# Kernel tuning notes

Hardware: AMD Instinct MI355X
Metric: run time of the kernel (lower is better)

## Reference

```python
import jax, jax.numpy as jnp
import numpy as np

N = 262144        # examples
N_RULES = 128     # weak labeling functions
D_L = 128         # extra feature dim of x_l
NHIDDEN = 256
NCLASS = 10
NFEAT = N_RULES + D_L


def setup_inputs() -> dict:
    key = jax.random.key(0)
    k1, k2, k3, k4 = jax.random.split(key, 4)
    # weak-rule votes: -1 = abstain, 0..NCLASS-1 = class vote (stored as float, as in torch)
    x_lf = jax.random.randint(k1, (N, N_RULES), -1, NCLASS).astype(jnp.float32)
    x_l = jax.random.normal(k2, (N, D_L), dtype=jnp.float32)
    W1 = jax.random.normal(k3, (NFEAT, NHIDDEN), dtype=jnp.float32) / np.sqrt(NFEAT).astype(np.float32)
    b1 = jnp.zeros((NHIDDEN,), jnp.float32)
    W2 = jax.random.normal(k4, (NHIDDEN, N_RULES), dtype=jnp.float32) / np.sqrt(NHIDDEN).astype(np.float32)
    b2 = jnp.zeros((N_RULES,), jnp.float32)
    return {"x_lf": x_lf, "x_l": x_l, "W1": W1, "b1": b1, "W2": W2, "b2": b2}


def reference(x_lf, x_l, W1, b1, W2, b2):
    # MLP attention scores over rules
    x = jnp.concatenate([x_lf, x_l], axis=1)            # (N, NFEAT)
    z = jnp.tanh(x @ W1 + b1) @ W2 + b2                 # (N, N_RULES)
    score = jax.nn.softmax(z, axis=1)                   # (N, N_RULES)
    mask = (x_lf >= 0).astype(score.dtype)
    coverage_score = score * mask                       # (N, N_RULES)
    # bucket-sum of scores by voted class (single-pass scatter-add instead of
    # the original O(nclass) masked-reduction loop); abstains (-1) -> bucket NCLASS, dropped
    idx = jnp.where(x_lf >= 0, x_lf.astype(jnp.int32), NCLASS)  # (N, N_RULES)
    score_matrix = jax.vmap(
        lambda s, i: jax.ops.segment_sum(s, i, num_segments=NCLASS + 1)
    )(score, idx)[:, :NCLASS]                           # (N, NCLASS)
    softmax_new_y = jax.nn.log_softmax(score_matrix, axis=1)
    return softmax_new_y, coverage_score
```

## Files before the change

### kernel.cpp

```cpp
#include <hip/hip_runtime.h>
#include <hip/hip_bf16.h>

#define NRULES 128
#define NH 256
#define NC 10
#define NF 256
#define BM 128

typedef __attribute__((ext_vector_type(8))) __bf16 bf16x8;
typedef __attribute__((ext_vector_type(4))) __bf16 bf16x4;
typedef __attribute__((ext_vector_type(4))) float f32x4;
typedef __attribute__((ext_vector_type(4))) int i32x4;

static __device__ __forceinline__ unsigned int f2bf_bits(float f) {
    unsigned int u = __float_as_uint(f);
    u += 0x7fffu + ((u >> 16) & 1u);
    return u >> 16;
}

static __device__ __forceinline__ float tanh_fast(float x) {
    float xc = fminf(fmaxf(x, -15.f), 15.f);
    float e = __expf(2.f * xc);
    return 1.f - 2.f * __builtin_amdgcn_rcpf(e + 1.f);
}

__global__ __launch_bounds__(256) void prep_transpose(
    const float* __restrict__ W1, const float* __restrict__ W2,
    unsigned short* __restrict__ W1T, unsigned short* __restrict__ W2T)
{
    __shared__ float tile[64][65];
    const int b = blockIdx.x;
    const float* src;
    unsigned short* dst;
    int sstride;
    if (b < 16) {
        int ti = b >> 2, tj = b & 3;
        src = W1 + ti * 64 * 256 + tj * 64;  sstride = 256;
        dst = W1T + tj * 64 * 256 + ti * 64;
    } else {
        int bb = b - 16;
        int ti = bb >> 1, tj = bb & 1;
        src = W2 + ti * 64 * 128 + tj * 64;  sstride = 128;
        dst = W2T + tj * 64 * 256 + ti * 64;
    }
    const int t = threadIdx.x;
    #pragma unroll
    for (int i = 0; i < 4; ++i) {
        int idx = i * 256 + t;
        int r = idx >> 4, c4 = (idx & 15) * 4;
        f32x4 v = *(const f32x4*)(src + r * sstride + c4);
        tile[r][c4 + 0] = v.x; tile[r][c4 + 1] = v.y;
        tile[r][c4 + 2] = v.z; tile[r][c4 + 3] = v.w;
    }
    __syncthreads();
    #pragma unroll
    for (int i = 0; i < 2; ++i) {
        int idx = i * 256 + t;
        int rr = idx >> 3, cc = (idx & 7) * 8;
        i32x4 pk;
        #pragma unroll
        for (int j = 0; j < 4; ++j) {
            unsigned int lo = f2bf_bits(tile[cc + 2 * j][rr]);
            unsigned int hi = f2bf_bits(tile[cc + 2 * j + 1][rr]);
            pk[j] = (int)(lo | (hi << 16));
        }
        *(i32x4*)(dst + rr * 256 + cc) = pk;
    }
}

__global__ __launch_bounds__(512, 4) void fused_mlp_attn(
    const float* __restrict__ x_lf, const float* __restrict__ x_l,
    const float* __restrict__ b1, const float* __restrict__ b2,
    const unsigned short* __restrict__ W1T, const unsigned short* __restrict__ W2T,
    float* __restrict__ out0, float* __restrict__ out1)
{
    __shared__ __align__(16) unsigned char smem[BM * 512 + BM * 68];
    unsigned char* Xs = smem;
    unsigned char* Vs = smem + BM * 512;

    const int tid = threadIdx.x;
    const long e0 = (long)blockIdx.x * BM;

    #pragma unroll
    for (int i = 0; i < 8; ++i) {
        int idx = i * 512 + tid;
        int e = idx >> 5;
        int c = idx & 31;
        const float* src = (c < 16) ? (x_lf + (e0 + e) * 128 + c * 8)
                                    : (x_l  + (e0 + e) * 128 + (c - 16) * 8);
        f32x4 a  = *(const f32x4*)src;
        f32x4 bq = *(const f32x4*)(src + 4);
        bf16x8 pk;
        pk[0] = (__bf16)a.x;  pk[1] = (__bf16)a.y;
        pk[2] = (__bf16)a.z;  pk[3] = (__bf16)a.w;
        pk[4] = (__bf16)bq.x; pk[5] = (__bf16)bq.y;
        pk[6] = (__bf16)bq.z; pk[7] = (__bf16)bq.w;
        *(bf16x8*)(Xs + e * 512 + ((c ^ (e & 7)) << 4)) = pk;
        if (c < 16) {
            unsigned int v = 0;
            v |= (unsigned int)((int)a.x  + 1);
            v |= (unsigned int)((int)a.y  + 1) << 4;
            v |= (unsigned int)((int)a.z  + 1) << 8;
            v |= (unsigned int)((int)a.w  + 1) << 12;
            v |= (unsigned int)((int)bq.x + 1) << 16;
            v |= (unsigned int)((int)bq.y + 1) << 20;
            v |= (unsigned int)((int)bq.z + 1) << 24;
            v |= (unsigned int)((int)bq.w + 1) << 28;
            *(unsigned int*)(Vs + e * 68 + c * 4) = v;
        }
    }
    __syncthreads();

    const int wv  = tid >> 6;
    const int lane = tid & 63;
    const int q   = lane >> 4;
    const int l15 = lane & 15;

    const int hb = wv * 32;
    f32x4 acc[2][8];
    #pragma unroll
    for (int mt = 0; mt < 2; ++mt)
        #pragma unroll
        for (int nt = 0; nt < 8; ++nt)
            acc[mt][nt] = (f32x4){0.f, 0.f, 0.f, 0.f};

    for (int kk = 0; kk < 8; ++kk) {
        const int k = kk * 32 + q * 8;
        bf16x8 af[2];
        #pragma unroll
        for (int mt = 0; mt < 2; ++mt)
            af[mt] = *(const bf16x8*)(W1T + (hb + mt * 16 + l15) * 256 + k);
        const int cc = kk * 4 + q;
        bf16x8 bfq[8];
        #pragma unroll
        for (int nt = 0; nt < 8; ++nt) {
            int e = nt * 16 + l15;
            bfq[nt] = *(const bf16x8*)(Xs + e * 512 + ((cc ^ (e & 7)) << 4));
        }
        #pragma unroll
        for (int mt = 0; mt < 2; ++mt)
            #pragma unroll
            for (int nt = 0; nt < 8; ++nt)
                acc[mt][nt] = __builtin_amdgcn_mfma_f32_16x16x32_bf16(
                    af[mt], bfq[nt], acc[mt][nt], 0, 0, 0);
    }

    #pragma unroll
    for (int mt = 0; mt < 2; ++mt) {
        f32x4 bv = *(const f32x4*)(b1 + hb + mt * 16 + q * 4);
        #pragma unroll
        for (int nt = 0; nt < 8; ++nt)
            #pragma unroll
            for (int j = 0; j < 4; ++j)
                acc[mt][nt][j] = tanh_fast(acc[mt][nt][j] + bv[j]);
    }

    __syncthreads();

    #pragma unroll
    for (int mt = 0; mt < 2; ++mt) {
        int h = hb + mt * 16 + q * 4;
        int c16 = h >> 3;
        int sub = (h & 4) << 1;
        #pragma unroll
        for (int nt = 0; nt < 8; ++nt) {
            int e = nt * 16 + l15;
            bf16x4 d;
            d[0] = (__bf16)acc[mt][nt][0]; d[1] = (__bf16)acc[mt][nt][1];
            d[2] = (__bf16)acc[mt][nt][2]; d[3] = (__bf16)acc[mt][nt][3];
            *(bf16x4*)(Xs + e * 512 + ((c16 ^ (e & 7)) << 4) + sub) = d;
        }
    }
    __syncthreads();

    const int eb = wv * 16;
    f32x4 acc2[8];
    #pragma unroll
    for (int mt = 0; mt < 8; ++mt)
        acc2[mt] = (f32x4){0.f, 0.f, 0.f, 0.f};

    for (int kk = 0; kk < 8; ++kk) {
        const int k = kk * 32 + q * 8;
        bf16x8 af2[8];
        #pragma unroll
        for (int mt = 0; mt < 8; ++mt)
            af2[mt] = *(const bf16x8*)(W2T + (mt * 16 + l15) * 256 + k);
        const int cc = kk * 4 + q;
        int e = eb + l15;
        bf16x8 bf2 = *(const bf16x8*)(Xs + e * 512 + ((cc ^ (e & 7)) << 4));
        #pragma unroll
        for (int mt = 0; mt < 8; ++mt)
            acc2[mt] = __builtin_amdgcn_mfma_f32_16x16x32_bf16(
                af2[mt], bf2, acc2[mt], 0, 0, 0);
    }

    {
        const int e = eb + l15;

        #pragma unroll
        for (int mt = 0; mt < 8; ++mt) {
            f32x4 bv = *(const f32x4*)(b2 + mt * 16 + q * 4);
            acc2[mt] += bv;
        }

        int vt[8];
        #pragma unroll
        for (int mt = 0; mt < 8; ++mt)
            vt[mt] = *(const unsigned short*)(Vs + e * 68 + mt * 8 + q * 2);

        float m = -3.4e38f;
        #pragma unroll
        for (int mt = 0; mt < 8; ++mt)
            #pragma unroll
            for (int j = 0; j < 4; ++j)
                m = fmaxf(m, acc2[mt][j]);
        m = fmaxf(m, __shfl_xor(m, 16));
        m = fmaxf(m, __shfl_xor(m, 32));

        float s = 0.f;
        #pragma unroll
        for (int mt = 0; mt < 8; ++mt)
            #pragma unroll
            for (int j = 0; j < 4; ++j) {
                float p = __expf(acc2[mt][j] - m);
                acc2[mt][j] = p;
                s += p;
            }
        s += __shfl_xor(s, 16);
        s += __shfl_xor(s, 32);
        const float inv = __builtin_amdgcn_rcpf(s);

        float bucket[NC];
        #pragma unroll
        for (int c = 0; c < NC; ++c) bucket[c] = 0.f;

        #pragma unroll
        for (int mt = 0; mt < 8; ++mt) {
            int u = vt[mt];
            f32x4 cov;
            #pragma unroll
            for (int j = 0; j < 4; ++j) {
                float sc = acc2[mt][j] * inv;
                int v = (u >> (4 * j)) & 15;
                cov[j] = (v != 0) ? sc : 0.f;
                #pragma unroll
                for (int c = 0; c < NC; ++c)
                    bucket[c] += (v == c + 1) ? sc : 0.f;
            }
            *(f32x4*)(out1 + (e0 + e) * 128 + mt * 16 + q * 4) = cov;
        }

        #pragma unroll
        for (int c = 0; c < NC; ++c) {
            bucket[c] += __shfl_xor(bucket[c], 16);
            bucket[c] += __shfl_xor(bucket[c], 32);
        }

        float m10 = bucket[0];
        #pragma unroll
        for (int c = 1; c < NC; ++c) m10 = fmaxf(m10, bucket[c]);
        float se = 0.f;
        #pragma unroll
        for (int c = 0; c < NC; ++c) se += __expf(bucket[c] - m10);
        const float lse = m10 + __logf(se);

        if (q == 0) {
            float* o = out0 + (e0 + e) * 10;
            #pragma unroll
            for (int c = 0; c < NC; ++c) o[c] = bucket[c] - lse;
        }
    }
}

extern "C" void kernel_launch(void* const* d_in, const int* in_sizes, int n_in,
                              void* d_out, int out_size, void* d_ws, size_t ws_size,
                              hipStream_t stream)
{
    const float* x_lf = (const float*)d_in[0];
    const float* x_l  = (const float*)d_in[1];
    const float* W1   = (const float*)d_in[2];
    const float* b1   = (const float*)d_in[3];
    const float* W2   = (const float*)d_in[4];
    const float* b2   = (const float*)d_in[5];
    const int n = in_sizes[0] / NRULES;
    float* out0 = (float*)d_out;
    float* out1 = out0 + (long)n * NC;
    unsigned short* W1T = (unsigned short*)d_ws;
    unsigned short* W2T = W1T + NH * NF;

    prep_transpose<<<24, 256, 0, stream>>>(W1, W2, W1T, W2T);
    fused_mlp_attn<<<n / BM, 512, 0, stream>>>(x_lf, x_l, b1, b2, W1T, W2T,
                                               out0, out1);
}
```

Before: 479.0 us.

## Stage coverage output through LDS and bucket scores with shared-memory atomics

```diff
diff --git a/kernel.cpp b/kernel.cpp
--- a/kernel.cpp
+++ b/kernel.cpp
@@ -74,13 +74,21 @@
     const unsigned short* __restrict__ W1T, const unsigned short* __restrict__ W2T,
     float* __restrict__ out0, float* __restrict__ out1)
 {
-    __shared__ __align__(16) unsigned char smem[BM * 512 + BM * 68];
+    __shared__ __align__(16) unsigned char smem[BM * 512 + BM * 68 + BM * 40];
     unsigned char* Xs = smem;
     unsigned char* Vs = smem + BM * 512;
+    float* lbuck = (float*)(smem + BM * 512 + BM * 68);
 
     const int tid = threadIdx.x;
     const long e0 = (long)blockIdx.x * BM;
 
+    #pragma unroll
+    for (int i = 0; i < 3; ++i) {
+        int idx = i * 512 + tid;
+        if (idx < BM * 10) lbuck[idx] = 0.f;
+    }
+
+    f32x4 ra[8], rb[8];
     #pragma unroll
     for (int i = 0; i < 8; ++i) {
         int idx = i * 512 + tid;
@@ -88,8 +96,15 @@
         int c = idx & 31;
         const float* src = (c < 16) ? (x_lf + (e0 + e) * 128 + c * 8)
                                     : (x_l  + (e0 + e) * 128 + (c - 16) * 8);
-        f32x4 a  = *(const f32x4*)src;
-        f32x4 bq = *(const f32x4*)(src + 4);
+        ra[i] = *(const f32x4*)src;
+        rb[i] = *(const f32x4*)(src + 4);
+    }
+    #pragma unroll
+    for (int i = 0; i < 8; ++i) {
+        int idx = i * 512 + tid;
+        int e = idx >> 5;
+        int c = idx & 31;
+        f32x4 a = ra[i], bq = rb[i];
         bf16x8 pk;
         pk[0] = (__bf16)a.x;  pk[1] = (__bf16)a.y;
         pk[2] = (__bf16)a.z;  pk[3] = (__bf16)a.w;
@@ -194,9 +209,8 @@
                 af2[mt], bf2, acc2[mt], 0, 0, 0);
     }
 
+    const int e = eb + l15;
     {
-        const int e = eb + l15;
-
         #pragma unroll
         for (int mt = 0; mt < 8; ++mt) {
             f32x4 bv = *(const f32x4*)(b2 + mt * 16 + q * 4);
@@ -230,45 +244,48 @@
         s += __shfl_xor(s, 32);
         const float inv = __builtin_amdgcn_rcpf(s);
 
-        float bucket[NC];
-        #pragma unroll
-        for (int c = 0; c < NC; ++c) bucket[c] = 0.f;
-
         #pragma unroll
         for (int mt = 0; mt < 8; ++mt) {
             int u = vt[mt];
-            f32x4 cov;
             #pragma unroll
             for (int j = 0; j < 4; ++j) {
                 float sc = acc2[mt][j] * inv;
                 int v = (u >> (4 * j)) & 15;
-                cov[j] = (v != 0) ? sc : 0.f;
-                #pragma unroll
-                for (int c = 0; c < NC; ++c)
-                    bucket[c] += (v == c + 1) ? sc : 0.f;
+                acc2[mt][j] = (v != 0) ? sc : 0.f;
+                if (v != 0) atomicAdd(&lbuck[e * 10 + v - 1], sc);
             }
-            *(f32x4*)(out1 + (e0 + e) * 128 + mt * 16 + q * 4) = cov;
-        }
-
-        #pragma unroll
-        for (int c = 0; c < NC; ++c) {
-            bucket[c] += __shfl_xor(bucket[c], 16);
-            bucket[c] += __shfl_xor(bucket[c], 32);
-        }
-
-        float m10 = bucket[0];
-        #pragma unroll
-        for (int c = 1; c < NC; ++c) m10 = fmaxf(m10, bucket[c]);
+        }
+    }
+    __syncthreads();
+
+    #pragma unroll
+    for (int mt = 0; mt < 8; ++mt)
+        *(f32x4*)(Xs + e * 512 + (((mt * 4 + q) ^ (e & 7)) << 4)) = acc2[mt];
+    __syncthreads();
+
+    #pragma unroll
+    for (int i = 0; i < 8; ++i) {
+        int idx = i * 512 + tid;
+        int row = idx >> 5;
+        int ch  = idx & 31;
+        f32x4 vv = *(const f32x4*)(Xs + row * 512 + ((ch ^ (row & 7)) << 4));
+        __builtin_nontemporal_store(vv, (f32x4*)(out1 + e0 * 128 + (long)idx * 4));
+    }
+
+    if (tid < BM) {
+        float b[NC];
+        #pragma unroll
+        for (int c = 0; c < NC; ++c) b[c] = lbuck[tid * 10 + c];
+        float m10 = b[0];
+        #pragma unroll
+        for (int c = 1; c < NC; ++c) m10 = fmaxf(m10, b[c]);
         float se = 0.f;
         #pragma unroll
-        for (int c = 0; c < NC; ++c) se += __expf(bucket[c] - m10);
+        for (int c = 0; c < NC; ++c) se += __expf(b[c] - m10);
         const float lse = m10 + __logf(se);
-
-        if (q == 0) {
-            float* o = out0 + (e0 + e) * 10;
-            #pragma unroll
-            for (int c = 0; c < NC; ++c) o[c] = bucket[c] - lse;
-        }
+        float* o = out0 + (e0 + tid) * 10;
+        #pragma unroll
+        for (int c = 0; c < NC; ++c) o[c] = b[c] - lse;
     }
 }
 
```

Result: slower. 578.9 us (+20.9%).
